# Performance work log

Hardware: AMD Instinct MI355X
Metric: run time of the kernel (lower is better)

The kernel has to match this reference:

```python
import jax, jax.numpy as jnp
import numpy as np

HIDDEN = 64

def setup_inputs() -> dict:
    key = jax.random.key(0)
    ks = jax.random.split(key, 8)
    B, T, D, O, H = 1024, 256, 128, 128, HIDDEN
    s_ih = 1.0 / np.sqrt(H)
    inp = {
        "x": jax.random.normal(ks[0], (B, T, D), dtype=jnp.float32),
        "W_ih": jax.random.uniform(ks[1], (4 * H, D), jnp.float32, -s_ih, s_ih),
        "W_hh": jax.random.uniform(ks[2], (4 * H, H), jnp.float32, -s_ih, s_ih),
        "b_ih": jax.random.uniform(ks[3], (4 * H,), jnp.float32, -s_ih, s_ih),
        "b_hh": jax.random.uniform(ks[4], (4 * H,), jnp.float32, -s_ih, s_ih),
        "W_o": jax.random.uniform(ks[5], (O, H), jnp.float32, -s_ih, s_ih),
        "b_o": jax.random.uniform(ks[6], (O,), jnp.float32, -s_ih, s_ih),
    }
    return inp

def _lstm_last_h(x, W_ih, W_hh, b_ih, b_hh):
    # x: [B, T, D]. PyTorch gate order: i, f, g, o.
    B, T, D = x.shape
    H = HIDDEN
    # Precompute input contribution for all steps: [T, B, 4H]
    gx = jnp.einsum('btd,gd->tbg', x, W_ih) + (b_ih + b_hh)

    def step(carry, gx_t):
        h, c = carry
        gates = gx_t + h @ W_hh.T  # [B, 4H]
        i = jax.nn.sigmoid(gates[:, 0 * H:1 * H])
        f = jax.nn.sigmoid(gates[:, 1 * H:2 * H])
        g = jnp.tanh(gates[:, 2 * H:3 * H])
        o = jax.nn.sigmoid(gates[:, 3 * H:4 * H])
        c = f * c + i * g
        h = o * jnp.tanh(c)
        return (h, c), None

    h0 = jnp.zeros((B, H), x.dtype)
    c0 = jnp.zeros((B, H), x.dtype)
    (h_T, _), _ = jax.lax.scan(step, (h0, c0), gx)
    return h_T  # [B, H] == output[:, -1, :]

def reference(x, W_ih, W_hh, b_ih, b_hh, W_o, b_o):
    h = _lstm_last_h(x, W_ih, W_hh, b_ih, b_hh)
    logits = jax.nn.relu(h) @ W_o.T + b_o  # [B, O]; dropout is identity in eval
    return jax.nn.log_softmax(logits, axis=1)
```

## Files before the change

### kernel.cpp

```cpp
#include <hip/hip_runtime.h>
#include <math.h>

constexpr int B = 1024, T = 256, D = 128, H = 64, O = 128;
constexpr int BQ = 4;
constexpr int NBLK = B / BQ;
constexpr int TC = 8;
constexpr int NCH = T / TC;

typedef __attribute__((ext_vector_type(8))) short short8;
typedef __attribute__((ext_vector_type(4))) float f32x4;

__device__ __forceinline__ unsigned short f2bf(float f) {
    union { float f; unsigned u; } v; v.f = f;
    return (unsigned short)((v.u + 0x7FFF + ((v.u >> 16) & 1)) >> 16);
}
__device__ __forceinline__ float frcp(float x) { return __builtin_amdgcn_rcpf(x); }
__device__ __forceinline__ float sigmoidf_(float x) {
    return frcp(1.0f + __expf(-x));
}
__device__ __forceinline__ float tanhf_(float x) {
    return fmaf(2.0f, frcp(1.0f + __expf(-2.0f * x)), -1.0f);
}
__device__ __forceinline__ void lds_barrier() {
    asm volatile("s_waitcnt lgkmcnt(0)\n\ts_barrier" ::: "memory");
}

__global__ __launch_bounds__(256, 1)
void lstm_fused(const float* __restrict__ x, const float* __restrict__ Wih,
                const float* __restrict__ Whh, const float* __restrict__ bih,
                const float* __restrict__ bhh, const float* __restrict__ Wo,
                const float* __restrict__ bo, float* __restrict__ out)
{
    __shared__ unsigned short xfrag[2 * 2048];
    __shared__ unsigned short hfrag[2 * 4 * 96];
    __shared__ float hfin[4 * 64];

    const int tid  = threadIdx.x;
    const int lane = tid & 63;
    const int w    = tid >> 6;
    const int lq   = lane & 15;
    const int qd   = lane >> 4;
    const int b0   = blockIdx.x * BQ;

    short8 wih_f[4][4];
    short8 whh_f[4][2];
    float  bias[4];
    #pragma unroll
    for (int q = 0; q < 4; ++q) {
        const int n = 64 * q + 16 * w + lq;
        #pragma unroll
        for (int c = 0; c < 4; ++c) {
            const float* p = Wih + (size_t)n * D + 32 * c + 8 * qd;
            short8 v;
            #pragma unroll
            for (int j = 0; j < 8; ++j) v[j] = (short)f2bf(p[j]);
            wih_f[q][c] = v;
        }
        #pragma unroll
        for (int c = 0; c < 2; ++c) {
            const float* p = Whh + (size_t)n * H + 32 * c + 8 * qd;
            short8 v;
            #pragma unroll
            for (int j = 0; j < 8; ++j) v[j] = (short)f2bf(p[j]);
            whh_f[q][c] = v;
        }
        bias[q] = bih[n] + bhh[n];
    }

    const int ms    = tid >> 4;
    const int kslot = tid & 15;
    const int c_p   = kslot >> 2;
    const int q_p   = kslot & 3;
    const int l_p   = (q_p << 4) | ms;
    const int xoff  = c_p * 1024 + ((l_p * 16) ^ (c_p * 32));
    const int bb    = ms >> 2, tsp = ms & 3;
    const float* xbase = x + (size_t)(b0 + bb) * T * D + 8 * kslot;

    int xro[4];
    #pragma unroll
    for (int c = 0; c < 4; ++c) xro[c] = c * 1024 + ((lane * 16) ^ (c * 32));

    for (int i = tid; i < 384; i += 256) ((unsigned int*)hfrag)[i] = 0;

    float4 pf[2][2];

    #pragma unroll
    for (int g = 0; g < 2; ++g) {
        const float* p = xbase + (size_t)(4 * g + tsp) * D;
        pf[g][0] = *(const float4*)p;
        pf[g][1] = *(const float4*)(p + 4);
    }
    #pragma unroll
    for (int g = 0; g < 2; ++g) {
        float4 a = pf[g][0], bv = pf[g][1];
        short8 v;
        v[0] = (short)f2bf(a.x);  v[1] = (short)f2bf(a.y);
        v[2] = (short)f2bf(a.z);  v[3] = (short)f2bf(a.w);
        v[4] = (short)f2bf(bv.x); v[5] = (short)f2bf(bv.y);
        v[6] = (short)f2bf(bv.z); v[7] = (short)f2bf(bv.w);
        *(short8*)((char*)xfrag + g * 4096 + xoff) = v;
    }
    #pragma unroll
    for (int g = 0; g < 2; ++g) {
        const float* p = xbase + (size_t)(TC + 4 * g + tsp) * D;
        pf[g][0] = *(const float4*)p;
        pf[g][1] = *(const float4*)(p + 4);
    }
    __syncthreads();

    float gxr[TC][4];

    auto gx_burst = [&]() {
        #pragma unroll
        for (int g = 0; g < 2; ++g) {
            short8 xf[4];
            #pragma unroll
            for (int c = 0; c < 4; ++c)
                xf[c] = *(const short8*)((char*)xfrag + g * 4096 + xro[c]);
            #pragma unroll
            for (int q = 0; q < 4; ++q) {
                f32x4 a = {bias[q], bias[q], bias[q], bias[q]};
                #pragma unroll
                for (int c = 0; c < 4; ++c)
                    a = __builtin_amdgcn_mfma_f32_16x16x32_bf16(xf[c], wih_f[q][c], a, 0, 0, 0);
                #pragma unroll
                for (int r = 0; r < 4; ++r) gxr[4 * g + r][q] = a[r];
            }
        }
    };

    gx_burst();
    lds_barrier();
    #pragma unroll
    for (int g = 0; g < 2; ++g) {
        float4 a = pf[g][0], bv = pf[g][1];
        short8 v;
        v[0] = (short)f2bf(a.x);  v[1] = (short)f2bf(a.y);
        v[2] = (short)f2bf(a.z);  v[3] = (short)f2bf(a.w);
        v[4] = (short)f2bf(bv.x); v[5] = (short)f2bf(bv.y);
        v[6] = (short)f2bf(bv.z); v[7] = (short)f2bf(bv.w);
        *(short8*)((char*)xfrag + g * 4096 + xoff) = v;
    }
    #pragma unroll
    for (int g = 0; g < 2; ++g) {
        const float* p = xbase + (size_t)(2 * TC + 4 * g + tsp) * D;
        pf[g][0] = *(const float4*)p;
        pf[g][1] = *(const float4*)(p + 4);
    }

    float cst = 0.0f, hlast = 0.0f;

    for (int ch = 0; ch < NCH; ++ch) {
        #pragma unroll
        for (int tt = 0; tt < TC; ++tt) {
            const int hcur = tt & 1, hnxt = hcur ^ 1;

            short8 hfr[2];
            #pragma unroll
            for (int c = 0; c < 2; ++c)
                hfr[c] = *(const short8*)(hfrag + hcur * 384 +
                                          (lq >> 2) * 96 + 32 * c + 8 * qd);

            float gv[4];
            #pragma unroll
            for (int q = 0; q < 4; ++q) {
                f32x4 a = {gxr[tt][q], 0.0f, 0.0f, 0.0f};
                #pragma unroll
                for (int c = 0; c < 2; ++c)
                    a = __builtin_amdgcn_mfma_f32_16x16x32_bf16(hfr[c], whh_f[q][c], a, 0, 0, 0);
                gv[q] = a[0];
            }

            float gi = sigmoidf_(gv[0]);
            float gf = sigmoidf_(gv[1]);
            float gg = tanhf_  (gv[2]);
            float go = sigmoidf_(gv[3]);
            float c2 = fmaf(gf, cst, gi * gg);
            cst = c2;
            float hv = go * tanhf_(c2);
            hlast = hv;
            hfrag[hnxt * 384 + qd * 96 + 16 * w + lq] = f2bf(hv);

            lds_barrier();
        }

        if (ch + 1 < NCH) {
            gx_burst();
            lds_barrier();
            #pragma unroll
            for (int g = 0; g < 2; ++g) {
                float4 a = pf[g][0], bv = pf[g][1];
                short8 v;
                v[0] = (short)f2bf(a.x);  v[1] = (short)f2bf(a.y);
                v[2] = (short)f2bf(a.z);  v[3] = (short)f2bf(a.w);
                v[4] = (short)f2bf(bv.x); v[5] = (short)f2bf(bv.y);
                v[6] = (short)f2bf(bv.z); v[7] = (short)f2bf(bv.w);
                *(short8*)((char*)xfrag + g * 4096 + xoff) = v;
            }
            const int ch3 = (ch + 3 < NCH) ? ch + 3 : NCH - 1;
            #pragma unroll
            for (int g = 0; g < 2; ++g) {
                const float* p = xbase + ((size_t)ch3 * TC + 4 * g + tsp) * D;
                pf[g][0] = *(const float4*)p;
                pf[g][1] = *(const float4*)(p + 4);
            }
        }
    }

    hfin[qd * 64 + 16 * w + lq] = hlast;
    __syncthreads();

    {
        const int m = w;
        float l0 = bo[lane], l1 = bo[lane + 64];
        const float* w0 = Wo + (size_t)lane * H;
        const float* w1 = Wo + (size_t)(lane + 64) * H;
        #pragma unroll
        for (int k = 0; k < H; ++k) {
            float rh = fmaxf(hfin[m * 64 + k], 0.0f);
            l0 += rh * w0[k];
            l1 += rh * w1[k];
        }
        float mx = fmaxf(l0, l1);
        #pragma unroll
        for (int sh = 32; sh > 0; sh >>= 1) mx = fmaxf(mx, __shfl_xor(mx, sh));
        float e = __expf(l0 - mx) + __expf(l1 - mx);
        #pragma unroll
        for (int sh = 32; sh > 0; sh >>= 1) e += __shfl_xor(e, sh);
        float lse = mx + __logf(e);
        float* op = out + (size_t)(b0 + m) * O;
        op[lane]      = l0 - lse;
        op[lane + 64] = l1 - lse;
    }
}

extern "C" void kernel_launch(void* const* d_in, const int* in_sizes, int n_in,
                              void* d_out, int out_size, void* d_ws, size_t ws_size,
                              hipStream_t stream) {
    const float* x   = (const float*)d_in[0];
    const float* Wih = (const float*)d_in[1];
    const float* Whh = (const float*)d_in[2];
    const float* bih = (const float*)d_in[3];
    const float* bhh = (const float*)d_in[4];
    const float* Wo  = (const float*)d_in[5];
    const float* bo  = (const float*)d_in[6];
    lstm_fused<<<dim3(NBLK), dim3(256), 0, stream>>>(
        x, Wih, Whh, bih, bhh, Wo, bo, (float*)d_out);
}
```

Measured before the change: 297.7 us.

## Give each wavefront its own batch row to remove per-step block barriers

Restructures the LSTM so each wavefront owns one batch element and computes all 256 gate columns itself. It keeps the full W_hh in registers (16x2 fragments) and stages W_ih in swizzled LDS. The block-wide barrier after every timestep goes away, and h is exchanged only within a wave through LDS. The input projection is computed per 16-step chunk into LDS and read back into registers. The cost is much higher register pressure and LDS footprint, plus redundant MFMA work: each wave runs 32 MFMAs per step on a single real row.

```diff
diff --git a/kernel.cpp b/kernel.cpp
--- a/kernel.cpp
+++ b/kernel.cpp
@@ -4,7 +4,7 @@
 constexpr int B = 1024, T = 256, D = 128, H = 64, O = 128;
 constexpr int BQ = 4;
 constexpr int NBLK = B / BQ;
-constexpr int TC = 8;
+constexpr int TC = 16;
 constexpr int NCH = T / TC;
 
 typedef __attribute__((ext_vector_type(8))) short short8;
@@ -20,9 +20,6 @@
 }
 __device__ __forceinline__ float tanhf_(float x) {
     return fmaf(2.0f, frcp(1.0f + __expf(-2.0f * x)), -1.0f);
-}
-__device__ __forceinline__ void lds_barrier() {
-    asm volatile("s_waitcnt lgkmcnt(0)\n\ts_barrier" ::: "memory");
 }
 
 __global__ __launch_bounds__(256, 1)
@@ -31,195 +28,169 @@
                 const float* __restrict__ bhh, const float* __restrict__ Wo,
                 const float* __restrict__ bo, float* __restrict__ out)
 {
-    __shared__ unsigned short xfrag[2 * 2048];
-    __shared__ unsigned short hfrag[2 * 4 * 96];
-    __shared__ float hfin[4 * 64];
+    __shared__ unsigned short wihlds[256 * 128];
+    __shared__ float gxlds[4][16 * 320];
+    __shared__ unsigned short hlds[4][64];
+    __shared__ float hfin[4][64];
 
     const int tid  = threadIdx.x;
     const int lane = tid & 63;
     const int w    = tid >> 6;
     const int lq   = lane & 15;
     const int qd   = lane >> 4;
-    const int b0   = blockIdx.x * BQ;
-
-    short8 wih_f[4][4];
-    short8 whh_f[4][2];
-    float  bias[4];
+    const int b    = blockIdx.x * BQ + w;
+
+    #pragma unroll
+    for (int i = 0; i < 16; ++i) {
+        int gid = i * 256 + tid;
+        int n = gid >> 4, kg = gid & 15;
+        const float* p = Wih + (size_t)n * D + 8 * kg;
+        short8 v;
+        #pragma unroll
+        for (int j = 0; j < 8; ++j) v[j] = (short)f2bf(p[j]);
+        *(short8*)((char*)wihlds + n * 256 + ((kg ^ (n & 15)) << 4)) = v;
+    }
+
+    short8 whh_f[16][2];
+    #pragma unroll
+    for (int t16 = 0; t16 < 16; ++t16)
+        #pragma unroll
+        for (int c = 0; c < 2; ++c) {
+            const float* p = Whh + (size_t)(16 * t16 + lq) * H + 32 * c + 8 * qd;
+            short8 v;
+            #pragma unroll
+            for (int j = 0; j < 8; ++j) v[j] = (short)f2bf(p[j]);
+            whh_f[t16][c] = v;
+        }
+
+    float bias4[4];
     #pragma unroll
     for (int q = 0; q < 4; ++q) {
-        const int n = 64 * q + 16 * w + lq;
+        int n = 64 * q + 16 * qd + lq;
+        bias4[q] = bih[n] + bhh[n];
+    }
+
+    __syncthreads();
+
+    const float* xb = x + (size_t)b * T * D + (size_t)lq * D + 8 * qd;
+    float4 pf[8];
+    auto issue_pf = [&](int t0) {
         #pragma unroll
         for (int c = 0; c < 4; ++c) {
-            const float* p = Wih + (size_t)n * D + 32 * c + 8 * qd;
+            const float* p = xb + (size_t)t0 * D + 32 * c;
+            pf[2 * c]     = *(const float4*)p;
+            pf[2 * c + 1] = *(const float4*)(p + 4);
+        }
+    };
+    short8 xf[4];
+    auto cvt_xf = [&]() {
+        #pragma unroll
+        for (int c = 0; c < 4; ++c) {
+            float4 a = pf[2 * c], bv = pf[2 * c + 1];
             short8 v;
-            #pragma unroll
-            for (int j = 0; j < 8; ++j) v[j] = (short)f2bf(p[j]);
-            wih_f[q][c] = v;
-        }
-        #pragma unroll
-        for (int c = 0; c < 2; ++c) {
-            const float* p = Whh + (size_t)n * H + 32 * c + 8 * qd;
-            short8 v;
-            #pragma unroll
-            for (int j = 0; j < 8; ++j) v[j] = (short)f2bf(p[j]);
-            whh_f[q][c] = v;
-        }
-        bias[q] = bih[n] + bhh[n];
-    }
-
-    const int ms    = tid >> 4;
-    const int kslot = tid & 15;
-    const int c_p   = kslot >> 2;
-    const int q_p   = kslot & 3;
-    const int l_p   = (q_p << 4) | ms;
-    const int xoff  = c_p * 1024 + ((l_p * 16) ^ (c_p * 32));
-    const int bb    = ms >> 2, tsp = ms & 3;
-    const float* xbase = x + (size_t)(b0 + bb) * T * D + 8 * kslot;
-
-    int xro[4];
-    #pragma unroll
-    for (int c = 0; c < 4; ++c) xro[c] = c * 1024 + ((lane * 16) ^ (c * 32));
-
-    for (int i = tid; i < 384; i += 256) ((unsigned int*)hfrag)[i] = 0;
-
-    float4 pf[2][2];
-
-    #pragma unroll
-    for (int g = 0; g < 2; ++g) {
-        const float* p = xbase + (size_t)(4 * g + tsp) * D;
-        pf[g][0] = *(const float4*)p;
-        pf[g][1] = *(const float4*)(p + 4);
-    }
-    #pragma unroll
-    for (int g = 0; g < 2; ++g) {
-        float4 a = pf[g][0], bv = pf[g][1];
-        short8 v;
-        v[0] = (short)f2bf(a.x);  v[1] = (short)f2bf(a.y);
-        v[2] = (short)f2bf(a.z);  v[3] = (short)f2bf(a.w);
-        v[4] = (short)f2bf(bv.x); v[5] = (short)f2bf(bv.y);
-        v[6] = (short)f2bf(bv.z); v[7] = (short)f2bf(bv.w);
-        *(short8*)((char*)xfrag + g * 4096 + xoff) = v;
-    }
-    #pragma unroll
-    for (int g = 0; g < 2; ++g) {
-        const float* p = xbase + (size_t)(TC + 4 * g + tsp) * D;
-        pf[g][0] = *(const float4*)p;
-        pf[g][1] = *(const float4*)(p + 4);
-    }
-    __syncthreads();
-
-    float gxr[TC][4];
-
-    auto gx_burst = [&]() {
-        #pragma unroll
-        for (int g = 0; g < 2; ++g) {
-            short8 xf[4];
-            #pragma unroll
-            for (int c = 0; c < 4; ++c)
-                xf[c] = *(const short8*)((char*)xfrag + g * 4096 + xro[c]);
+            v[0] = (short)f2bf(a.x);  v[1] = (short)f2bf(a.y);
+            v[2] = (short)f2bf(a.z);  v[3] = (short)f2bf(a.w);
+            v[4] = (short)f2bf(bv.x); v[5] = (short)f2bf(bv.y);
+            v[6] = (short)f2bf(bv.z); v[7] = (short)f2bf(bv.w);
+            xf[c] = v;
+        }
+    };
+
+    float* gxw = gxlds[w];
+    f32x4 gxq[4][4];
+
+    auto burst = [&]() {
+        #pragma unroll
+        for (int t16 = 0; t16 < 16; ++t16) {
+            f32x4 a = {0.f, 0.f, 0.f, 0.f};
+            #pragma unroll
+            for (int c = 0; c < 4; ++c) {
+                short8 bf = *(const short8*)((char*)wihlds +
+                              (16 * t16 + lq) * 256 + (((4 * c + qd) ^ lq) << 4));
+                a = __builtin_amdgcn_mfma_f32_16x16x32_bf16(xf[c], bf, a, 0, 0, 0);
+            }
+            *(f32x4*)&gxw[t16 * 320 + lq * 20 + 4 * qd] = a;
+        }
+    };
+    auto readback = [&]() {
+        #pragma unroll
+        for (int q = 0; q < 4; ++q)
+            #pragma unroll
+            for (int s = 0; s < 4; ++s) {
+                f32x4 v = *(const f32x4*)&gxw[(4 * q + qd) * 320 + lq * 20 + 4 * s];
+                v[0] += bias4[q]; v[1] += bias4[q];
+                v[2] += bias4[q]; v[3] += bias4[q];
+                gxq[q][s] = v;
+            }
+    };
+
+    unsigned short* hw = hlds[w];
+    if (lane < 32) ((unsigned int*)hw)[lane] = 0u;
+
+    f32x4 accq[16];
+    #pragma unroll
+    for (int i = 0; i < 16; ++i) accq[i] = (f32x4){0.f, 0.f, 0.f, 0.f};
+
+    issue_pf(0);
+    cvt_xf();
+    issue_pf(TC);
+    burst();
+    readback();
+
+    float cst = 0.0f, hv = 0.0f;
+
+    for (int ch = 0; ch < NCH; ++ch) {
+        #pragma unroll
+        for (int tt = 0; tt < TC; ++tt) {
+            short8 hfr0 = *(const short8*)((char*)hw + 16 * qd);
+            short8 hfr1 = *(const short8*)((char*)hw + 64 + 16 * qd);
+
+            float gv[4];
             #pragma unroll
             for (int q = 0; q < 4; ++q) {
-                f32x4 a = {bias[q], bias[q], bias[q], bias[q]};
+                const float g = gxq[q][tt >> 2][tt & 3];
                 #pragma unroll
-                for (int c = 0; c < 4; ++c)
-                    a = __builtin_amdgcn_mfma_f32_16x16x32_bf16(xf[c], wih_f[q][c], a, 0, 0, 0);
-                #pragma unroll
-                for (int r = 0; r < 4; ++r) gxr[4 * g + r][q] = a[r];
-            }
-        }
-    };
-
-    gx_burst();
-    lds_barrier();
-    #pragma unroll
-    for (int g = 0; g < 2; ++g) {
-        float4 a = pf[g][0], bv = pf[g][1];
-        short8 v;
-        v[0] = (short)f2bf(a.x);  v[1] = (short)f2bf(a.y);
-        v[2] = (short)f2bf(a.z);  v[3] = (short)f2bf(a.w);
-        v[4] = (short)f2bf(bv.x); v[5] = (short)f2bf(bv.y);
-        v[6] = (short)f2bf(bv.z); v[7] = (short)f2bf(bv.w);
-        *(short8*)((char*)xfrag + g * 4096 + xoff) = v;
-    }
-    #pragma unroll
-    for (int g = 0; g < 2; ++g) {
-        const float* p = xbase + (size_t)(2 * TC + 4 * g + tsp) * D;
-        pf[g][0] = *(const float4*)p;
-        pf[g][1] = *(const float4*)(p + 4);
-    }
-
-    float cst = 0.0f, hlast = 0.0f;
-
-    for (int ch = 0; ch < NCH; ++ch) {
-        #pragma unroll
-        for (int tt = 0; tt < TC; ++tt) {
-            const int hcur = tt & 1, hnxt = hcur ^ 1;
-
-            short8 hfr[2];
-            #pragma unroll
-            for (int c = 0; c < 2; ++c)
-                hfr[c] = *(const short8*)(hfrag + hcur * 384 +
-                                          (lq >> 2) * 96 + 32 * c + 8 * qd);
-
-            float gv[4];
-            #pragma unroll
-            for (int q = 0; q < 4; ++q) {
-                f32x4 a = {gxr[tt][q], 0.0f, 0.0f, 0.0f};
-                #pragma unroll
-                for (int c = 0; c < 2; ++c)
-                    a = __builtin_amdgcn_mfma_f32_16x16x32_bf16(hfr[c], whh_f[q][c], a, 0, 0, 0);
-                gv[q] = a[0];
+                for (int d = 0; d < 4; ++d) {
+                    const int i = 4 * q + d;
+                    accq[i][0] = g;
+                    accq[i] = __builtin_amdgcn_mfma_f32_16x16x32_bf16(
+                                  hfr0, whh_f[i][0], accq[i], 0, 0, 0);
+                    accq[i] = __builtin_amdgcn_mfma_f32_16x16x32_bf16(
+                                  hfr1, whh_f[i][1], accq[i], 0, 0, 0);
+                }
+                float v01 = (qd & 1) ? accq[4 * q + 1][0] : accq[4 * q + 0][0];
+                float v23 = (qd & 1) ? accq[4 * q + 3][0] : accq[4 * q + 2][0];
+                gv[q] = (qd & 2) ? v23 : v01;
             }
 
             float gi = sigmoidf_(gv[0]);
             float gf = sigmoidf_(gv[1]);
             float gg = tanhf_  (gv[2]);
             float go = sigmoidf_(gv[3]);
-            float c2 = fmaf(gf, cst, gi * gg);
-            cst = c2;
-            float hv = go * tanhf_(c2);
-            hlast = hv;
-            hfrag[hnxt * 384 + qd * 96 + 16 * w + lq] = f2bf(hv);
-
-            lds_barrier();
+            cst = fmaf(gf, cst, gi * gg);
+            hv  = go * tanhf_(cst);
+            hw[16 * qd + lq] = f2bf(hv);
         }
 
         if (ch + 1 < NCH) {
-            gx_burst();
-            lds_barrier();
-            #pragma unroll
-            for (int g = 0; g < 2; ++g) {
-                float4 a = pf[g][0], bv = pf[g][1];
-                short8 v;
-                v[0] = (short)f2bf(a.x);  v[1] = (short)f2bf(a.y);
-                v[2] = (short)f2bf(a.z);  v[3] = (short)f2bf(a.w);
-                v[4] = (short)f2bf(bv.x); v[5] = (short)f2bf(bv.y);
-                v[6] = (short)f2bf(bv.z); v[7] = (short)f2bf(bv.w);
-                *(short8*)((char*)xfrag + g * 4096 + xoff) = v;
-            }
-            const int ch3 = (ch + 3 < NCH) ? ch + 3 : NCH - 1;
-            #pragma unroll
-            for (int g = 0; g < 2; ++g) {
-                const float* p = xbase + ((size_t)ch3 * TC + 4 * g + tsp) * D;
-                pf[g][0] = *(const float4*)p;
-                pf[g][1] = *(const float4*)(p + 4);
-            }
-        }
-    }
-
-    hfin[qd * 64 + 16 * w + lq] = hlast;
-    __syncthreads();
-
+            cvt_xf();
+            const int tnext = (ch + 2 < NCH ? ch + 2 : NCH - 1) * TC;
+            issue_pf(tnext);
+            burst();
+            readback();
+        }
+    }
+
+    hfin[w][16 * qd + lq] = hv;
     {
-        const int m = w;
         float l0 = bo[lane], l1 = bo[lane + 64];
         const float* w0 = Wo + (size_t)lane * H;
         const float* w1 = Wo + (size_t)(lane + 64) * H;
         #pragma unroll
         for (int k = 0; k < H; ++k) {
-            float rh = fmaxf(hfin[m * 64 + k], 0.0f);
-            l0 += rh * w0[k];
-            l1 += rh * w1[k];
+            float rh = fmaxf(hfin[w][k], 0.0f);
+            l0 = fmaf(rh, w0[k], l0);
+            l1 = fmaf(rh, w1[k], l1);
         }
         float mx = fmaxf(l0, l1);
         #pragma unroll
@@ -228,7 +199,7 @@
         #pragma unroll
         for (int sh = 32; sh > 0; sh >>= 1) e += __shfl_xor(e, sh);
         float lse = mx + __logf(e);
-        float* op = out + (size_t)(b0 + m) * O;
+        float* op = out + (size_t)b * O;
         op[lane]      = l0 - lse;
         op[lane + 64] = l1 - lse;
     }
```

New measurement: 398.7 us. +33.9%, slower.
